# Kernel tuning notes

Measured on AMD Instinct MI355X. Metric: run time of the kernel, lower is better.

## Reference

```python
import jax, jax.numpy as jnp
import numpy as np

ROPE_BASE = 100.0  # croco/dust3r RoPE2D default freq


def _rope1d(tok, pos1d, base=ROPE_BASE):
    # tok: [B,H,N,D], pos1d: [B,N] int
    D = tok.shape[-1]
    half = D // 2
    inv_freq = 1.0 / (base ** (jnp.arange(0, D, 2, dtype=jnp.float32) / D))  # [D/2]
    ang = pos1d[..., None].astype(jnp.float32) * inv_freq                    # [B,N,D/2]
    ang = jnp.concatenate([ang, ang], axis=-1)                               # [B,N,D]
    cos = jnp.cos(ang)[:, None, :, :].astype(tok.dtype)  # [B,1,N,D]
    sin = jnp.sin(ang)[:, None, :, :].astype(tok.dtype)
    t1, t2 = tok[..., :half], tok[..., half:]
    rot = jnp.concatenate([-t2, t1], axis=-1)  # rotate_half
    return tok * cos + rot * sin


def rope2d(tok, pos, base=ROPE_BASE):
    # tok: [B,H,N,C], pos: [B,N,2] (y,x) integer coords
    D = tok.shape[-1] // 2
    y = _rope1d(tok[..., :D], pos[..., 0], base)
    x = _rope1d(tok[..., D:], pos[..., 1], base)
    return jnp.concatenate([y, x], axis=-1)


def setup_inputs() -> dict:
    key = jax.random.key(0)
    k1, k2, k3, k4, k5 = jax.random.split(key, 5)
    B, H, N, C = 2, 12, 2049, 64
    q = jax.random.normal(k1, (B, H, N, C), dtype=jnp.float32)
    k = jax.random.normal(k2, (B, H, N, C), dtype=jnp.float32)
    v = jax.random.normal(k3, (B, H, N, C), dtype=jnp.float32)
    qpos = jax.random.randint(k4, (B, N, 2), 0, 64, dtype=jnp.int32)
    kpos = jax.random.randint(k5, (B, N, 2), 0, 64, dtype=jnp.int32)
    mask_for_attention = jnp.ones((B, N, N), dtype=bool)
    return {"q": q, "k": k, "v": v, "qpos": qpos, "kpos": kpos,
            "mask_for_attention": mask_for_attention, "num_cls": 1}


def reference(q, k, v, qpos, kpos, mask_for_attention, num_cls):
    B, H, Nq, C = q.shape
    scale = C ** -0.5
    # split off cls tokens, apply RoPE only to positional tokens
    q_nc = rope2d(q[:, :, num_cls:], qpos[:, num_cls:])
    k_nc = rope2d(k[:, :, num_cls:], kpos[:, num_cls:])
    # block similarity matrix:
    #            | K_cls |   K_pos    |
    #   | Q_cls |        sim_qcls_k   |
    #   |       | sim_q |-------------|
    #   | Q_pos |        |  sim_rope  |
    sim_rope = jnp.einsum('bhqc,bhkc->bhqk', q_nc, k_nc)                      # [B,H,Nq-cls,Nk-cls]
    sim_qcls_k = jnp.einsum('bhqc,bhkc->bhqk', q[:, :, :num_cls], k[:, :, num_cls:])
    sim_q = jnp.einsum('bhqc,bhkc->bhqk', q, k[:, :, :num_cls])               # [B,H,Nq,cls]
    sim = jnp.concatenate([sim_qcls_k, sim_rope], axis=-2)
    sim = jnp.concatenate([sim_q, sim], axis=-1)                              # [B,H,Nq,Nk]
    sim = sim * scale
    sim = jnp.where(mask_for_attention[:, None], sim, -jnp.inf)
    attn = jax.nn.softmax(sim, axis=-1)
    x = jnp.einsum('bhqk,bhkc->bhqc', attn, v)
    return x.transpose(0, 2, 1, 3).reshape(B, Nq, C * H)
```

## Files before the change

### kernel.cpp

```cpp
#include <hip/hip_runtime.h>
#include <hip/hip_bf16.h>

typedef __attribute__((ext_vector_type(8))) short bf16x8;
typedef __attribute__((ext_vector_type(16))) float f32x16;
typedef __attribute__((ext_vector_type(4))) float f32x4;
typedef __attribute__((ext_vector_type(2))) float f32x2;
typedef unsigned short u16;

#define BN 2
#define HN 12
#define NN 2049
#define CN 64
#define NT 2048
#define BH 24
#define QSCL 0.1803368801111204f

__device__ __forceinline__ u16 f2bf(float x) {
  unsigned u = __builtin_bit_cast(unsigned, x);
  unsigned r = (u + 0x7fffu + ((u >> 16) & 1u)) >> 16;
  return (u16)r;
}

__device__ __forceinline__ unsigned cvt_pk(float lo, float hi) {
  unsigned r;
  asm("v_cvt_pk_bf16_f32 %0, %1, %2" : "=v"(r) : "v"(lo), "v"(hi));
  return r;
}

union PU {
  unsigned u[4];
  bf16x8 v;
};
union B8 {
  f32x2 h[2];
  bf16x8 v;
};

__global__ __launch_bounds__(256) void rope_pack(
    const float* __restrict__ q, const float* __restrict__ k, const float* __restrict__ v,
    const int* __restrict__ qpos, const int* __restrict__ kpos,
    u16* __restrict__ Qr, u16* __restrict__ Kr, u16* __restrict__ Vt,
    float* __restrict__ S0, float* __restrict__ Pl, float* __restrict__ Po) {
  const int bh = blockIdx.x;
  const int t = blockIdx.y;
  const int b = bh / HN;
  const int tid = threadIdx.x;
  const int wv = tid >> 6, l = tid & 63;

  __shared__ float lutc[1024], luts[1024];
  __shared__ u16 ldsV[64][36];
  __shared__ float q0s[64], k0s[64];
  __shared__ float osum[4][64];
  __shared__ float psum[4];

  const int n0 = 1 + t * 32;
  const size_t base0 = (size_t)bh * NN * CN;

  const float LF = 6.6438561897747253f / 16.0f;
  for (int i = tid; i < 1024; i += 256) {
    const int pos = i >> 4, f = i & 15;
    const float inv = exp2f(-(float)f * LF);
    float sv, cv;
    sincosf((float)pos * inv, &sv, &cv);
    lutc[i] = cv;
    luts[i] = sv;
  }
  if (tid < 64) {
    q0s[tid] = q[base0 + tid];
    k0s[tid] = k[base0 + tid];
  }
  __syncthreads();

  float oacc = 0.f, pacc = 0.f;
#pragma unroll 2
  for (int i = 0; i < 8; ++i) {
    const int tok = i * 4 + wv;
    const int c = l;
    const int n = n0 + tok;
    const size_t base = base0 + (size_t)n * CN;
    const int cp = c & 31, f = cp & 15, axis = c >> 5;
    const int qp_ = qpos[((size_t)b * NN + n) * 2 + axis];
    const int kp_ = kpos[((size_t)b * NN + n) * 2 + axis];
    const float qa = q[base + c];
    const float ka = k[base + c];
    const float qrot = (cp < 16) ? -q[base + c + 16] : q[base + c - 16];
    const float krot = (cp < 16) ? -k[base + c + 16] : k[base + c - 16];
    Qr[((size_t)bh * NT + (n - 1)) * CN + c] =
        f2bf((qa * lutc[qp_ * 16 + f] + qrot * luts[qp_ * 16 + f]) * QSCL);
    Kr[((size_t)bh * NT + (n - 1)) * CN + c] =
        f2bf(ka * lutc[kp_ * 16 + f] + krot * luts[kp_ * 16 + f]);
    const float vv = v[base + c];
    ldsV[c][tok] = f2bf(vv);

    float pk = ka * q0s[c];
    float pq = qa * k0s[c];
    pk += __shfl_xor(pk, 1, 64);  pq += __shfl_xor(pq, 1, 64);
    pk += __shfl_xor(pk, 2, 64);  pq += __shfl_xor(pq, 2, 64);
    pk += __shfl_xor(pk, 4, 64);  pq += __shfl_xor(pq, 4, 64);
    pk += __shfl_xor(pk, 8, 64);  pq += __shfl_xor(pq, 8, 64);
    pk += __shfl_xor(pk, 16, 64); pq += __shfl_xor(pq, 16, 64);
    pk += __shfl_xor(pk, 32, 64); pq += __shfl_xor(pq, 32, 64);
    const float p = __builtin_amdgcn_exp2f(pk * QSCL);
    pacc += p;
    oacc += p * vv;
    if (l == 0) S0[(size_t)bh * NT + (n - 1)] = pq * QSCL;
  }
  osum[wv][l] = oacc;
  if (l == 0) psum[wv] = pacc;
  __syncthreads();

  for (int e = tid; e < 2048; e += 256) {
    const int c = e >> 5, tok = e & 31;
    Vt[((size_t)bh * CN + c) * NT + (t * 32 + tok)] = ldsV[c][tok];
  }
  if (tid < 64)
    Po[(size_t)(bh * 64 + t) * 64 + tid] =
        osum[0][tid] + osum[1][tid] + osum[2][tid] + osum[3][tid];
  if (tid == 0) Pl[bh * 64 + t] = psum[0] + psum[1] + psum[2] + psum[3];
}

__global__ __launch_bounds__(64) void row0_reduce(
    const float* __restrict__ q, const float* __restrict__ k, const float* __restrict__ v,
    const float* __restrict__ Pl, const float* __restrict__ Po, float* __restrict__ out) {
  const int bh = blockIdx.x;
  const int b = bh / HN, h = bh % HN;
  const int c = threadIdx.x;
  const size_t base0 = (size_t)bh * NN * CN;
  float pr = q[base0 + c] * k[base0 + c];
  pr += __shfl_xor(pr, 1, 64);
  pr += __shfl_xor(pr, 2, 64);
  pr += __shfl_xor(pr, 4, 64);
  pr += __shfl_xor(pr, 8, 64);
  pr += __shfl_xor(pr, 16, 64);
  pr += __shfl_xor(pr, 32, 64);
  const float p00 = __builtin_amdgcn_exp2f(pr * QSCL);
  float L = p00;
  float acc = p00 * v[base0 + c];
#pragma unroll
  for (int i = 0; i < 64; ++i) {
    L += Pl[bh * 64 + i];
    acc += Po[(size_t)(bh * 64 + i) * 64 + c];
  }
  out[(size_t)b * NN * (HN * CN) + h * CN + c] = acc / L;
}

__global__ __launch_bounds__(256, 3) void attn_main(
    const float* __restrict__ v,
    const u16* __restrict__ Qr, const u16* __restrict__ Kr, const u16* __restrict__ Vt,
    const float* __restrict__ S0, float* __restrict__ out) {
  const int wg = blockIdx.x;
  const int bh = 3 * (wg & 7) + ((wg >> 3) >> 5);
  const int qt = (wg >> 3) & 31;
  const int b = bh / HN, h = bh % HN;
  const int tid = threadIdx.x;
  const int wv = tid >> 6, l = tid & 63;
  const int l31 = l & 31, lh = l >> 5;
  const int qh = wv & 1, kh = wv >> 1;

  __shared__ u16 ldsK[2][4096];
  __shared__ u16 ldsV[2][4096];
  __shared__ float v0f[64];
  __shared__ float Lbuf[64];
  float* Obuf = reinterpret_cast<float*>(&ldsK[0][0]);

  if (tid < 64) v0f[tid] = v[(size_t)bh * NN * CN + tid];
  __syncthreads();

  const int qrow = qt * 64 + qh * 32 + l31;
  const u16* qp = Qr + ((size_t)bh * NT + qrow) * CN + lh * 8;
  bf16x8 qf[4];
#pragma unroll
  for (int s = 0; s < 4; ++s) qf[s] = *reinterpret_cast<const bf16x8*>(qp + s * 16);

  const float s0l2 = S0[(size_t)bh * NT + qrow];
  const float p0 = __builtin_amdgcn_exp2f(s0l2);
  const float l0 = (kh == 0) ? p0 : 0.f;

  PU onesu;
  onesu.u[0] = onesu.u[1] = onesu.u[2] = onesu.u[3] = 0x3F803F80u;

  f32x16 o[2], Lacc;
#pragma unroll
  for (int reg = 0; reg < 16; ++reg) Lacc[reg] = 0.f;
#pragma unroll
  for (int half = 0; half < 2; ++half)
#pragma unroll
    for (int reg = 0; reg < 16; ++reg)
      o[half][reg] =
          (kh == 0) ? p0 * v0f[(reg & 3) + 8 * (reg >> 2) + 4 * lh + 32 * half] : 0.f;

  const u16* Kbh = Kr + (size_t)bh * NT * CN;
  const u16* Vbh = Vt + (size_t)bh * CN * NT;
  char* ldsKc = reinterpret_cast<char*>(&ldsK[0][0]);
  char* ldsVc = reinterpret_cast<char*>(&ldsV[0][0]);

  const int s16 = tid & 7, srowA = tid >> 3, srowB = (tid >> 3) + 32;
  const int swA = (srowA & 15) << 3, swB = (srowB & 15) << 3;
  const int kA0 = srowA * 128 + ((s16 * 16) ^ swA);
  const int kA1 = srowA * 128 + ((s16 * 16 + 8) ^ swA);
  const int kB0 = srowB * 128 + ((s16 * 16) ^ swB);
  const int kB1 = srowB * 128 + ((s16 * 16 + 8) ^ swB);
  const int vb1 = 32 * (s16 >> 1) + 8 * (s16 & 1);
  const int vb2 = vb1 + 16;
  const int vA0 = srowA * 128 + (vb1 ^ swA);
  const int vA1 = srowA * 128 + (vb2 ^ swA);
  const int vB0 = srowB * 128 + (vb1 ^ swB);
  const int vB1 = srowB * 128 + (vb2 ^ swB);

  f32x4 kreg[2], vrg[2];
#define LOAD_TILE(nx)                                                                       \
  do {                                                                                      \
    kreg[0] = *reinterpret_cast<const f32x4*>(Kbh + (size_t)((nx) + srowA) * CN + s16 * 8); \
    kreg[1] = *reinterpret_cast<const f32x4*>(Kbh + (size_t)((nx) + srowB) * CN + s16 * 8); \
    vrg[0] = *reinterpret_cast<const f32x4*>(Vbh + (size_t)srowA * NT + (nx) + s16 * 8);    \
    vrg[1] = *reinterpret_cast<const f32x4*>(Vbh + (size_t)srowB * NT + (nx) + s16 * 8);    \
  } while (0)

#define WR2(base, off, vec4)                                                  \
  do {                                                                        \
    f32x2 lo_, hi_;                                                           \
    lo_[0] = (vec4)[0]; lo_[1] = (vec4)[1];                                   \
    hi_[0] = (vec4)[2]; hi_[1] = (vec4)[3];                                   \
    *reinterpret_cast<f32x2*>((base) + (off##0)) = lo_;                       \
    *reinterpret_cast<f32x2*>((base) + (off##1)) = hi_;                       \
  } while (0)

#define STAGE_WRITE(bofs)               \
  do {                                  \
    WR2(ldsKc + (bofs), kA, kreg[0]);   \
    WR2(ldsKc + (bofs), kB, kreg[1]);   \
    WR2(ldsVc + (bofs), vA, vrg[0]);    \
    WR2(ldsVc + (bofs), vB, vrg[1]);    \
  } while (0)

  LOAD_TILE(0);
  STAGE_WRITE(0);
  LOAD_TILE(64);

#pragma unroll 2
  for (int kt = 0; kt < 32; ++kt) {
    const int cur = (kt & 1) * 8192;
    const int nxt = ((kt + 1) & 1) * 8192;
    asm volatile("s_waitcnt lgkmcnt(0)" ::: "memory");
    __builtin_amdgcn_s_barrier();
    asm volatile("" ::: "memory");

    const int trow = kh * 32 + l31;
    const int tsw = (trow & 15) << 3;
    B8 kb[4];
#pragma unroll
    for (int st = 0; st < 4; ++st) {
      const int cb = st * 32 + lh * 16;
      kb[st].h[0] = *reinterpret_cast<const f32x2*>(ldsKc + cur + trow * 128 + (cb ^ tsw));
      kb[st].h[1] =
          *reinterpret_cast<const f32x2*>(ldsKc + cur + trow * 128 + ((cb + 8) ^ tsw));
    }
    f32x16 S;
#pragma unroll
    for (int reg = 0; reg < 16; ++reg) S[reg] = 0.f;
    __builtin_amdgcn_s_setprio(1);
#pragma unroll
    for (int st = 0; st < 4; ++st)
      S = __builtin_amdgcn_mfma_f32_32x32x16_bf16(kb[st].v, qf[st], S, 0, 0, 0);
    __builtin_amdgcn_s_setprio(0);

    if (kt < 31) {
      STAGE_WRITE(nxt);
      if (kt < 30) LOAD_TILE((kt + 2) * 64);
    }

    PU pa[2];
    {
      float e[16];
#pragma unroll
      for (int reg = 0; reg < 16; ++reg) e[reg] = __builtin_amdgcn_exp2f(S[reg]);
#pragma unroll
      for (int m = 0; m < 4; ++m) {
        pa[0].u[m] = cvt_pk(e[2 * m], e[2 * m + 1]);
        pa[1].u[m] = cvt_pk(e[8 + 2 * m], e[9 + 2 * m]);
      }
    }

    __builtin_amdgcn_s_setprio(1);
#pragma unroll
    for (int half = 0; half < 2; ++half) {
      const int crow = half * 32 + l31;
      const int csw = (crow & 15) << 3;
#pragma unroll
      for (int ks = 0; ks < 2; ++ks) {
        B8 vb;
        const int pb = (kh * 2 + ks) * 32 + lh * 16;
        vb.h[0] = *reinterpret_cast<const f32x2*>(ldsVc + cur + crow * 128 + (pb ^ csw));
        vb.h[1] = *reinterpret_cast<const f32x2*>(ldsVc + cur + crow * 128 + ((pb + 8) ^ csw));
        o[half] = __builtin_amdgcn_mfma_f32_32x32x16_bf16(vb.v, pa[ks].v, o[half], 0, 0, 0);
      }
    }
    Lacc = __builtin_amdgcn_mfma_f32_32x32x16_bf16(onesu.v, pa[0].v, Lacc, 0, 0, 0);
    Lacc = __builtin_amdgcn_mfma_f32_32x32x16_bf16(onesu.v, pa[1].v, Lacc, 0, 0, 0);
    __builtin_amdgcn_s_setprio(0);
  }

  const float wls = Lacc[0] + l0;
  __syncthreads();
  if (kh == 1) {
#pragma unroll
    for (int half = 0; half < 2; ++half)
#pragma unroll
      for (int reg = 0; reg < 16; ++reg) {
        const int c = (reg & 3) + 8 * (reg >> 2) + 4 * lh + 32 * half;
        Obuf[qh * 2048 + c * 32 + l31] = o[half][reg];
      }
    if (lh == 0) Lbuf[qh * 32 + l31] = wls;
  }
  __syncthreads();
  if (kh == 0) {
    const float L = wls + Lbuf[qh * 32 + l31];
    const float invl = 1.0f / L;
    const int n = 1 + qrow;
    float* op = out + ((size_t)b * NN + n) * (HN * CN) + h * CN;
#pragma unroll
    for (int half = 0; half < 2; ++half) {
#pragma unroll
      for (int rg = 0; rg < 4; ++rg) {
        f32x4 val;
#pragma unroll
        for (int j = 0; j < 4; ++j) {
          const int reg = 4 * rg + j;
          const int c = (reg & 3) + 8 * (reg >> 2) + 4 * lh + 32 * half;
          val[j] = (o[half][reg] + Obuf[qh * 2048 + c * 32 + l31]) * invl;
        }
        *reinterpret_cast<f32x4*>(op + 8 * rg + 4 * lh + 32 * half) = val;
      }
    }
  }
#undef LOAD_TILE
#undef WR2
#undef STAGE_WRITE
}

extern "C" void kernel_launch(void* const* d_in, const int* in_sizes, int n_in,
                              void* d_out, int out_size, void* d_ws, size_t ws_size,
                              hipStream_t stream) {
  const float* q = (const float*)d_in[0];
  const float* k = (const float*)d_in[1];
  const float* v = (const float*)d_in[2];
  const int* qpos = (const int*)d_in[3];
  const int* kpos = (const int*)d_in[4];
  float* out = (float*)d_out;

  u16* Qr = (u16*)d_ws;
  u16* Kr = Qr + (size_t)BH * NT * CN;
  u16* Vt = Kr + (size_t)BH * NT * CN;
  float* S0 = (float*)(Vt + (size_t)BH * NT * CN);
  float* Pl = S0 + (size_t)BH * NT;
  float* Po = Pl + BH * 64;

  rope_pack<<<dim3(BH, 64), 256, 0, stream>>>(q, k, v, qpos, kpos, Qr, Kr, Vt, S0, Pl, Po);
  attn_main<<<dim3(BH * 32), 256, 0, stream>>>(v, Qr, Kr, Vt, S0, out);
  row0_reduce<<<dim3(BH), 64, 0, stream>>>(q, k, v, Pl, Po, out);
}
```

Baseline: 63.18 us.

## Software-pipeline PV MFMA one tile behind QK and drop ones-MFMA row sum

Restructures the attention main loop so each iteration issues the P·V MFMAs for the previous tile alongside the QK MFMAs for the current tile. The exp/pack latency can then overlap with matrix work, and a barrier is added before the staging write to protect the buffer still being read. It also replaces the two per-tile MFMAs against a ones matrix, used for the softmax denominator, with an fp32 scalar sum plus a cross-lane shuffle. The costs are an extra barrier per tile, more live registers for the V fragments, and a denominator summed from fp32 rather than bf16-rounded values.

```diff
diff --git a/kernel.cpp b/kernel.cpp
--- a/kernel.cpp
+++ b/kernel.cpp
@@ -175,13 +175,9 @@
   const float s0l2 = S0[(size_t)bh * NT + qrow];
   const float p0 = __builtin_amdgcn_exp2f(s0l2);
   const float l0 = (kh == 0) ? p0 : 0.f;
-
-  PU onesu;
-  onesu.u[0] = onesu.u[1] = onesu.u[2] = onesu.u[3] = 0x3F803F80u;
-
-  f32x16 o[2], Lacc;
-#pragma unroll
-  for (int reg = 0; reg < 16; ++reg) Lacc[reg] = 0.f;
+  float lsum = 0.f;
+
+  f32x16 o[2];
 #pragma unroll
   for (int half = 0; half < 2; ++half)
 #pragma unroll
@@ -207,6 +203,9 @@
   const int vB0 = srowB * 128 + (vb1 ^ swB);
   const int vB1 = srowB * 128 + (vb2 ^ swB);
 
+  const int trow = kh * 32 + l31;
+  const int tsw = (trow & 15) << 3;
+
   f32x4 kreg[2], vrg[2];
 #define LOAD_TILE(nx)                                                                       \
   do {                                                                                      \
@@ -233,74 +232,121 @@
     WR2(ldsVc + (bofs), vB, vrg[1]);    \
   } while (0)
 
+#define READ_K(kb, bofs)                                                                     \
+  do {                                                                                       \
+    _Pragma("unroll") for (int st = 0; st < 4; ++st) {                                       \
+      const int cb = st * 32 + lh * 16;                                                      \
+      kb[st].h[0] = *reinterpret_cast<const f32x2*>(ldsKc + (bofs) + trow * 128 + (cb ^ tsw));\
+      kb[st].h[1] =                                                                          \
+          *reinterpret_cast<const f32x2*>(ldsKc + (bofs) + trow * 128 + ((cb + 8) ^ tsw));   \
+    }                                                                                        \
+  } while (0)
+
+#define READ_V(vf, bofs)                                                                     \
+  do {                                                                                       \
+    _Pragma("unroll") for (int half = 0; half < 2; ++half) {                                 \
+      const int crow = half * 32 + l31;                                                      \
+      const int csw = (crow & 15) << 3;                                                      \
+      _Pragma("unroll") for (int ks = 0; ks < 2; ++ks) {                                     \
+        const int pb = (kh * 2 + ks) * 32 + lh * 16;                                         \
+        vf[half * 2 + ks].h[0] =                                                             \
+            *reinterpret_cast<const f32x2*>(ldsVc + (bofs) + crow * 128 + (pb ^ csw));       \
+        vf[half * 2 + ks].h[1] =                                                             \
+            *reinterpret_cast<const f32x2*>(ldsVc + (bofs) + crow * 128 + ((pb + 8) ^ csw)); \
+      }                                                                                      \
+    }                                                                                        \
+  } while (0)
+
+#define EXP_PACK(S, pa)                                                        \
+  do {                                                                         \
+    float e[16];                                                               \
+    _Pragma("unroll") for (int r2 = 0; r2 < 16; ++r2)                          \
+        e[r2] = __builtin_amdgcn_exp2f(S[r2]);                                 \
+    _Pragma("unroll") for (int r2 = 0; r2 < 16; r2 += 4)                       \
+        lsum += (e[r2] + e[r2 + 1]) + (e[r2 + 2] + e[r2 + 3]);                 \
+    _Pragma("unroll") for (int m = 0; m < 4; ++m) {                            \
+      pa[0].u[m] = cvt_pk(e[2 * m], e[2 * m + 1]);                             \
+      pa[1].u[m] = cvt_pk(e[8 + 2 * m], e[9 + 2 * m]);                         \
+    }                                                                          \
+  } while (0)
+
   LOAD_TILE(0);
   STAGE_WRITE(0);
   LOAD_TILE(64);
 
-#pragma unroll 2
-  for (int kt = 0; kt < 32; ++kt) {
+  PU pa[2];
+
+  asm volatile("s_waitcnt lgkmcnt(0)" ::: "memory");
+  __builtin_amdgcn_s_barrier();
+  asm volatile("" ::: "memory");
+  {
+    B8 kb[4];
+    READ_K(kb, 0);
+    f32x16 S;
+#pragma unroll
+    for (int reg = 0; reg < 16; ++reg) S[reg] = 0.f;
+    __builtin_amdgcn_s_setprio(1);
+#pragma unroll
+    for (int st = 0; st < 4; ++st)
+      S = __builtin_amdgcn_mfma_f32_32x32x16_bf16(kb[st].v, qf[st], S, 0, 0, 0);
+    __builtin_amdgcn_s_setprio(0);
+    EXP_PACK(S, pa);
+  }
+  __builtin_amdgcn_s_barrier();
+  asm volatile("" ::: "memory");
+  STAGE_WRITE(8192);
+  LOAD_TILE(128);
+
+  for (int kt = 1; kt < 32; ++kt) {
     const int cur = (kt & 1) * 8192;
-    const int nxt = ((kt + 1) & 1) * 8192;
+    const int prv = ((kt + 1) & 1) * 8192;
     asm volatile("s_waitcnt lgkmcnt(0)" ::: "memory");
     __builtin_amdgcn_s_barrier();
     asm volatile("" ::: "memory");
 
-    const int trow = kh * 32 + l31;
-    const int tsw = (trow & 15) << 3;
-    B8 kb[4];
-#pragma unroll
-    for (int st = 0; st < 4; ++st) {
-      const int cb = st * 32 + lh * 16;
-      kb[st].h[0] = *reinterpret_cast<const f32x2*>(ldsKc + cur + trow * 128 + (cb ^ tsw));
-      kb[st].h[1] =
-          *reinterpret_cast<const f32x2*>(ldsKc + cur + trow * 128 + ((cb + 8) ^ tsw));
-    }
+    B8 vf[4], kb[4];
+    READ_V(vf, prv);
+    READ_K(kb, cur);
+
+    __builtin_amdgcn_s_setprio(1);
+#pragma unroll
+    for (int half = 0; half < 2; ++half)
+#pragma unroll
+      for (int ks = 0; ks < 2; ++ks)
+        o[half] =
+            __builtin_amdgcn_mfma_f32_32x32x16_bf16(vf[half * 2 + ks].v, pa[ks].v, o[half], 0, 0, 0);
     f32x16 S;
 #pragma unroll
     for (int reg = 0; reg < 16; ++reg) S[reg] = 0.f;
-    __builtin_amdgcn_s_setprio(1);
 #pragma unroll
     for (int st = 0; st < 4; ++st)
       S = __builtin_amdgcn_mfma_f32_32x32x16_bf16(kb[st].v, qf[st], S, 0, 0, 0);
     __builtin_amdgcn_s_setprio(0);
 
+    EXP_PACK(S, pa);
+
+    __builtin_amdgcn_s_barrier();
+    asm volatile("" ::: "memory");
     if (kt < 31) {
-      STAGE_WRITE(nxt);
+      STAGE_WRITE(prv);
       if (kt < 30) LOAD_TILE((kt + 2) * 64);
     }
-
-    PU pa[2];
-    {
-      float e[16];
-#pragma unroll
-      for (int reg = 0; reg < 16; ++reg) e[reg] = __builtin_amdgcn_exp2f(S[reg]);
-#pragma unroll
-      for (int m = 0; m < 4; ++m) {
-        pa[0].u[m] = cvt_pk(e[2 * m], e[2 * m + 1]);
-        pa[1].u[m] = cvt_pk(e[8 + 2 * m], e[9 + 2 * m]);
-      }
-    }
-
+  }
+
+  {
+    B8 vf[4];
+    READ_V(vf, 8192);
     __builtin_amdgcn_s_setprio(1);
 #pragma unroll
-    for (int half = 0; half < 2; ++half) {
-      const int crow = half * 32 + l31;
-      const int csw = (crow & 15) << 3;
-#pragma unroll
-      for (int ks = 0; ks < 2; ++ks) {
-        B8 vb;
-        const int pb = (kh * 2 + ks) * 32 + lh * 16;
-        vb.h[0] = *reinterpret_cast<const f32x2*>(ldsVc + cur + crow * 128 + (pb ^ csw));
-        vb.h[1] = *reinterpret_cast<const f32x2*>(ldsVc + cur + crow * 128 + ((pb + 8) ^ csw));
-        o[half] = __builtin_amdgcn_mfma_f32_32x32x16_bf16(vb.v, pa[ks].v, o[half], 0, 0, 0);
-      }
-    }
-    Lacc = __builtin_amdgcn_mfma_f32_32x32x16_bf16(onesu.v, pa[0].v, Lacc, 0, 0, 0);
-    Lacc = __builtin_amdgcn_mfma_f32_32x32x16_bf16(onesu.v, pa[1].v, Lacc, 0, 0, 0);
+    for (int half = 0; half < 2; ++half)
+#pragma unroll
+      for (int ks = 0; ks < 2; ++ks)
+        o[half] =
+            __builtin_amdgcn_mfma_f32_32x32x16_bf16(vf[half * 2 + ks].v, pa[ks].v, o[half], 0, 0, 0);
     __builtin_amdgcn_s_setprio(0);
   }
 
-  const float wls = Lacc[0] + l0;
+  const float wls = lsum + __shfl_xor(lsum, 32, 64) + l0;
   __syncthreads();
   if (kh == 1) {
 #pragma unroll
@@ -336,6 +382,9 @@
 #undef LOAD_TILE
 #undef WR2
 #undef STAGE_WRITE
+#undef READ_K
+#undef READ_V
+#undef EXP_PACK
 }
 
 extern "C" void kernel_launch(void* const* d_in, const int* in_sizes, int n_in,
```

Measured after the change: 64.45 us. +2.0%, slower.

## Load K/V MFMA fragments directly from global memory, drop LDS staging

Applied to the files above, without the earlier changes.

The attention main loop no longer stages K and V tiles through double-buffered shared memory with barriers. Each wave loads its bf16 MFMA operand fragments straight from global memory, and the prep kernel writes V in a permuted per-64-token order so the fragment loads are contiguous. The row-sum is now accumulated with scalar adds plus one cross-lane shuffle instead of two ones-matrix MFMAs, and the occupancy hint is raised to 4. This removes LDS traffic and per-tile barriers, at the cost of redundant global/L2 reads across waves and no explicit prefetch to hide load latency.

```diff
diff --git a/kernel.cpp b/kernel.cpp
--- a/kernel.cpp
+++ b/kernel.cpp
@@ -111,7 +111,10 @@
 
   for (int e = tid; e < 2048; e += 256) {
     const int c = e >> 5, tok = e & 31;
-    Vt[((size_t)bh * CN + c) * NT + (t * 32 + tok)] = ldsV[c][tok];
+    const int T = t * 32 + tok;
+    const int t6 = T & 63, ch = t6 >> 3, j = t6 & 7;
+    const int pos = 16 * (ch >> 1) + 4 * (ch & 1) + 8 * (j >> 2) + (j & 3);
+    Vt[((size_t)bh * CN + c) * NT + (T >> 6) * 64 + pos] = ldsV[c][tok];
   }
   if (tid < 64)
     Po[(size_t)(bh * 64 + t) * 64 + tid] =
@@ -144,7 +147,7 @@
   out[(size_t)b * NN * (HN * CN) + h * CN + c] = acc / L;
 }
 
-__global__ __launch_bounds__(256, 3) void attn_main(
+__global__ __launch_bounds__(256, 4) void attn_main(
     const float* __restrict__ v,
     const u16* __restrict__ Qr, const u16* __restrict__ Kr, const u16* __restrict__ Vt,
     const float* __restrict__ S0, float* __restrict__ out) {
@@ -157,11 +160,9 @@
   const int l31 = l & 31, lh = l >> 5;
   const int qh = wv & 1, kh = wv >> 1;
 
-  __shared__ u16 ldsK[2][4096];
-  __shared__ u16 ldsV[2][4096];
   __shared__ float v0f[64];
   __shared__ float Lbuf[64];
-  float* Obuf = reinterpret_cast<float*>(&ldsK[0][0]);
+  __shared__ float Obuf[2][2048];
 
   if (tid < 64) v0f[tid] = v[(size_t)bh * NN * CN + tid];
   __syncthreads();
@@ -175,13 +176,9 @@
   const float s0l2 = S0[(size_t)bh * NT + qrow];
   const float p0 = __builtin_amdgcn_exp2f(s0l2);
   const float l0 = (kh == 0) ? p0 : 0.f;
-
-  PU onesu;
-  onesu.u[0] = onesu.u[1] = onesu.u[2] = onesu.u[3] = 0x3F803F80u;
-
-  f32x16 o[2], Lacc;
-#pragma unroll
-  for (int reg = 0; reg < 16; ++reg) Lacc[reg] = 0.f;
+  float lsum = 0.f;
+
+  f32x16 o[2];
 #pragma unroll
   for (int half = 0; half < 2; ++half)
 #pragma unroll
@@ -189,72 +186,26 @@
       o[half][reg] =
           (kh == 0) ? p0 * v0f[(reg & 3) + 8 * (reg >> 2) + 4 * lh + 32 * half] : 0.f;
 
-  const u16* Kbh = Kr + (size_t)bh * NT * CN;
-  const u16* Vbh = Vt + (size_t)bh * CN * NT;
-  char* ldsKc = reinterpret_cast<char*>(&ldsK[0][0]);
-  char* ldsVc = reinterpret_cast<char*>(&ldsV[0][0]);
-
-  const int s16 = tid & 7, srowA = tid >> 3, srowB = (tid >> 3) + 32;
-  const int swA = (srowA & 15) << 3, swB = (srowB & 15) << 3;
-  const int kA0 = srowA * 128 + ((s16 * 16) ^ swA);
-  const int kA1 = srowA * 128 + ((s16 * 16 + 8) ^ swA);
-  const int kB0 = srowB * 128 + ((s16 * 16) ^ swB);
-  const int kB1 = srowB * 128 + ((s16 * 16 + 8) ^ swB);
-  const int vb1 = 32 * (s16 >> 1) + 8 * (s16 & 1);
-  const int vb2 = vb1 + 16;
-  const int vA0 = srowA * 128 + (vb1 ^ swA);
-  const int vA1 = srowA * 128 + (vb2 ^ swA);
-  const int vB0 = srowB * 128 + (vb1 ^ swB);
-  const int vB1 = srowB * 128 + (vb2 ^ swB);
-
-  f32x4 kreg[2], vrg[2];
-#define LOAD_TILE(nx)                                                                       \
-  do {                                                                                      \
-    kreg[0] = *reinterpret_cast<const f32x4*>(Kbh + (size_t)((nx) + srowA) * CN + s16 * 8); \
-    kreg[1] = *reinterpret_cast<const f32x4*>(Kbh + (size_t)((nx) + srowB) * CN + s16 * 8); \
-    vrg[0] = *reinterpret_cast<const f32x4*>(Vbh + (size_t)srowA * NT + (nx) + s16 * 8);    \
-    vrg[1] = *reinterpret_cast<const f32x4*>(Vbh + (size_t)srowB * NT + (nx) + s16 * 8);    \
-  } while (0)
-
-#define WR2(base, off, vec4)                                                  \
-  do {                                                                        \
-    f32x2 lo_, hi_;                                                           \
-    lo_[0] = (vec4)[0]; lo_[1] = (vec4)[1];                                   \
-    hi_[0] = (vec4)[2]; hi_[1] = (vec4)[3];                                   \
-    *reinterpret_cast<f32x2*>((base) + (off##0)) = lo_;                       \
-    *reinterpret_cast<f32x2*>((base) + (off##1)) = hi_;                       \
-  } while (0)
-
-#define STAGE_WRITE(bofs)               \
-  do {                                  \
-    WR2(ldsKc + (bofs), kA, kreg[0]);   \
-    WR2(ldsKc + (bofs), kB, kreg[1]);   \
-    WR2(ldsVc + (bofs), vA, vrg[0]);    \
-    WR2(ldsVc + (bofs), vB, vrg[1]);    \
-  } while (0)
-
-  LOAD_TILE(0);
-  STAGE_WRITE(0);
-  LOAD_TILE(64);
+  const int trow = kh * 32 + l31;
+  const u16* kfp = Kr + ((size_t)bh * NT + trow) * CN + lh * 8;
+  const u16* vfp0 = Vt + ((size_t)bh * CN + l31) * NT + kh * 32 + lh * 8;
+  const u16* vfp1 = vfp0 + (size_t)32 * NT;
 
 #pragma unroll 2
   for (int kt = 0; kt < 32; ++kt) {
-    const int cur = (kt & 1) * 8192;
-    const int nxt = ((kt + 1) & 1) * 8192;
-    asm volatile("s_waitcnt lgkmcnt(0)" ::: "memory");
-    __builtin_amdgcn_s_barrier();
-    asm volatile("" ::: "memory");
-
-    const int trow = kh * 32 + l31;
-    const int tsw = (trow & 15) << 3;
-    B8 kb[4];
-#pragma unroll
-    for (int st = 0; st < 4; ++st) {
-      const int cb = st * 32 + lh * 16;
-      kb[st].h[0] = *reinterpret_cast<const f32x2*>(ldsKc + cur + trow * 128 + (cb ^ tsw));
-      kb[st].h[1] =
-          *reinterpret_cast<const f32x2*>(ldsKc + cur + trow * 128 + ((cb + 8) ^ tsw));
+    const u16* kp = kfp + (size_t)(kt * 64) * CN;
+    const u16* vp0 = vfp0 + kt * 64;
+    const u16* vp1 = vfp1 + kt * 64;
+    B8 kb[4], vf[4];
+#pragma unroll
+    for (int st = 0; st < 4; ++st)
+      kb[st].v = *reinterpret_cast<const bf16x8*>(kp + st * 16);
+#pragma unroll
+    for (int ks = 0; ks < 2; ++ks) {
+      vf[0 * 2 + ks].v = *reinterpret_cast<const bf16x8*>(vp0 + ks * 16);
+      vf[1 * 2 + ks].v = *reinterpret_cast<const bf16x8*>(vp1 + ks * 16);
     }
+
     f32x16 S;
 #pragma unroll
     for (int reg = 0; reg < 16; ++reg) S[reg] = 0.f;
@@ -264,16 +215,14 @@
       S = __builtin_amdgcn_mfma_f32_32x32x16_bf16(kb[st].v, qf[st], S, 0, 0, 0);
     __builtin_amdgcn_s_setprio(0);
 
-    if (kt < 31) {
-      STAGE_WRITE(nxt);
-      if (kt < 30) LOAD_TILE((kt + 2) * 64);
-    }
-
     PU pa[2];
     {
       float e[16];
 #pragma unroll
-      for (int reg = 0; reg < 16; ++reg) e[reg] = __builtin_amdgcn_exp2f(S[reg]);
+      for (int r2 = 0; r2 < 16; ++r2) e[r2] = __builtin_amdgcn_exp2f(S[r2]);
+#pragma unroll
+      for (int r2 = 0; r2 < 16; r2 += 4)
+        lsum += (e[r2] + e[r2 + 1]) + (e[r2 + 2] + e[r2 + 3]);
 #pragma unroll
       for (int m = 0; m < 4; ++m) {
         pa[0].u[m] = cvt_pk(e[2 * m], e[2 * m + 1]);
@@ -283,32 +232,23 @@
 
     __builtin_amdgcn_s_setprio(1);
 #pragma unroll
-    for (int half = 0; half < 2; ++half) {
-      const int crow = half * 32 + l31;
-      const int csw = (crow & 15) << 3;
-#pragma unroll
-      for (int ks = 0; ks < 2; ++ks) {
-        B8 vb;
-        const int pb = (kh * 2 + ks) * 32 + lh * 16;
-        vb.h[0] = *reinterpret_cast<const f32x2*>(ldsVc + cur + crow * 128 + (pb ^ csw));
-        vb.h[1] = *reinterpret_cast<const f32x2*>(ldsVc + cur + crow * 128 + ((pb + 8) ^ csw));
-        o[half] = __builtin_amdgcn_mfma_f32_32x32x16_bf16(vb.v, pa[ks].v, o[half], 0, 0, 0);
-      }
-    }
-    Lacc = __builtin_amdgcn_mfma_f32_32x32x16_bf16(onesu.v, pa[0].v, Lacc, 0, 0, 0);
-    Lacc = __builtin_amdgcn_mfma_f32_32x32x16_bf16(onesu.v, pa[1].v, Lacc, 0, 0, 0);
+    for (int half = 0; half < 2; ++half)
+#pragma unroll
+      for (int ks = 0; ks < 2; ++ks)
+        o[half] = __builtin_amdgcn_mfma_f32_32x32x16_bf16(vf[half * 2 + ks].v, pa[ks].v,
+                                                          o[half], 0, 0, 0);
     __builtin_amdgcn_s_setprio(0);
   }
 
-  const float wls = Lacc[0] + l0;
-  __syncthreads();
+  const float wls = lsum + __shfl_xor(lsum, 32, 64) + l0;
+  float* Ob = &Obuf[0][0];
   if (kh == 1) {
 #pragma unroll
     for (int half = 0; half < 2; ++half)
 #pragma unroll
       for (int reg = 0; reg < 16; ++reg) {
         const int c = (reg & 3) + 8 * (reg >> 2) + 4 * lh + 32 * half;
-        Obuf[qh * 2048 + c * 32 + l31] = o[half][reg];
+        Ob[qh * 2048 + c * 32 + l31] = o[half][reg];
       }
     if (lh == 0) Lbuf[qh * 32 + l31] = wls;
   }
@@ -327,15 +267,12 @@
         for (int j = 0; j < 4; ++j) {
           const int reg = 4 * rg + j;
           const int c = (reg & 3) + 8 * (reg >> 2) + 4 * lh + 32 * half;
-          val[j] = (o[half][reg] + Obuf[qh * 2048 + c * 32 + l31]) * invl;
+          val[j] = (o[half][reg] + Ob[qh * 2048 + c * 32 + l31]) * invl;
         }
         *reinterpret_cast<f32x4*>(op + 8 * rg + 4 * lh + 32 * half) = val;
       }
     }
   }
-#undef LOAD_TILE
-#undef WR2
-#undef STAGE_WRITE
 }
 
 extern "C" void kernel_launch(void* const* d_in, const int* in_sizes, int n_in,
```

Result: slower. 112.3 us (+77.8%).
